# Optimization experiments

Measured on AMD Instinct MI355X. Metric: run time of the kernel, lower is better.

The kernel has to match this reference:

```python
import jax, jax.numpy as jnp
import numpy as np

EPS = 1e-5

def layer_norm(x, gamma, beta):
    mu = jnp.mean(x, axis=-1, keepdims=True)
    var = jnp.var(x, axis=-1, keepdims=True)
    return (x - mu) * jax.lax.rsqrt(var + EPS) * gamma + beta

def setup_inputs() -> dict:
    key = jax.random.key(0)
    ks = jax.random.split(key, 8)
    B, S, D, OUT = 32768, 6, 128, 1024
    return {
        "x": jax.random.normal(ks[0], (B, S, D), dtype=jnp.float32),
        "W_qkv": jax.random.normal(ks[1], (D, 3 * D), dtype=jnp.float32) * 0.02,
        "b_qkv": jnp.zeros((3 * D,), dtype=jnp.float32),
        "g1": jnp.ones((256,), dtype=jnp.float32),
        "be1": jnp.zeros((256,), dtype=jnp.float32),
        "W_fp": jax.random.normal(ks[2], (256, 256), dtype=jnp.float32) * 0.02,
        "b_fp": jnp.zeros((256,), dtype=jnp.float32),
        "g2": jnp.ones((512,), dtype=jnp.float32),
        "be2": jnp.zeros((512,), dtype=jnp.float32),
        "W_s": jax.random.normal(ks[3], (S * 512, OUT), dtype=jnp.float32) * 0.02,
        "b_s": jnp.zeros((OUT,), dtype=jnp.float32),
    }

def reference(x, W_qkv, b_qkv, g1, be1, W_fp, b_fp, g2, be2, W_s, b_s):
    D = 128
    qkv = x @ W_qkv + b_qkv                      # [B,6,384]
    Q, K, V = qkv[..., :D], qkv[..., D:2*D], qkv[..., 2*D:]
    # attention WITHOUT softmax, as in the original module
    attn = jnp.einsum('bqd,bkd->bqk', Q, K)      # [B,6,6]
    attn_result = jnp.einsum('bqk,bkd->bqd', attn, V)  # [B,6,128]
    m = jnp.concatenate([x, attn_result], axis=2)      # [B,6,256]
    n = layer_norm(m, g1, be1)
    n = n @ W_fp + b_fp                          # [B,6,256]
    f = jnp.concatenate([n, m], axis=2)          # [B,6,512]
    f = layer_norm(f, g2, be2)
    f = f.reshape(-1, 6 * 512)                   # [B,3072]
    out = jax.nn.relu(f @ W_s + b_s)             # [B,1024]
    return out
```

## Files before the change

### kernel.cpp

```cpp
#include <hip/hip_runtime.h>
#include <stdint.h>

typedef short bf16x8 __attribute__((ext_vector_type(8)));
typedef float f32x4 __attribute__((ext_vector_type(4)));

__device__ __forceinline__ float bf2f(uint16_t b){
  union { uint32_t u; float f; } v; v.u = ((uint32_t)b) << 16; return v.f;
}
__device__ __forceinline__ float u2f(uint32_t u){
  union { uint32_t u; float f; } v; v.u = u; return v.f;
}
__device__ __forceinline__ uint16_t f2bf(float f){
  union { float f; uint32_t u; } v; v.f = f;
  uint32_t u = v.u;
  return (uint16_t)((u + 0x7FFFu + ((u >> 16) & 1u)) >> 16);
}

__device__ __forceinline__ void gl2lds16(const uint16_t* g, uint16_t* l) {
  __builtin_amdgcn_global_load_lds((const __attribute__((address_space(1))) void*)g,
                                   (__attribute__((address_space(3))) void*)l, 16, 0, 0);
}

__global__ __launch_bounds__(256) void transpose_cvt(
    const float* __restrict__ src, uint16_t* __restrict__ dst, int K, int N)
{
  __shared__ float tile[32][33];
  int n0 = blockIdx.x * 32, k0 = blockIdx.y * 32;
  int tx = threadIdx.x & 31, ty = threadIdx.x >> 5;
  #pragma unroll
  for (int i = 0; i < 4; i++)
    tile[ty + 8*i][tx] = src[(size_t)(k0 + ty + 8*i) * N + n0 + tx];
  __syncthreads();
  #pragma unroll
  for (int i = 0; i < 4; i++)
    dst[(size_t)(n0 + ty + 8*i) * K + k0 + tx] = f2bf(tile[tx][ty + 8*i]);
}

#define LX 136
#define LQ 392
#define LNM 264

__global__ __launch_bounds__(256) void fused_mid(
    const float* __restrict__ X, const uint16_t* __restrict__ WqkvT,
    const float* __restrict__ bqkv, const float* __restrict__ g1,
    const float* __restrict__ be1, const uint16_t* __restrict__ WfpT,
    const float* __restrict__ bfp, const float* __restrict__ g2,
    const float* __restrict__ be2, uint16_t* __restrict__ F)
{
  __shared__ uint16_t xs[48 * LX];
  __shared__ uint16_t qs[48 * LQ];
  __shared__ uint16_t nm[48 * LNM];
  __shared__ float    sb[8 * 36];
  __shared__ float    smu[48], srs[48];
  int t = threadIdx.x;
  int lane = t & 63, wave = t >> 6;
  int lr = lane & 15, lh = lane >> 4;
  size_t r0 = (size_t)blockIdx.x * 48;

  for (int i = t; i < 768; i += 256) {
    int row = i >> 4, c = (i & 15) * 8;
    const float* g = X + (r0 + row) * 128 + c;
    f32x4 v0 = *(const f32x4*)g, v1 = *(const f32x4*)(g + 4);
    bf16x8 o;
    #pragma unroll
    for (int j = 0; j < 4; j++) { o[j] = (short)f2bf(v0[j]); o[4+j] = (short)f2bf(v1[j]); }
    *(bf16x8*)(xs + row * LX + c) = o;
  }
  __syncthreads();

  {
    f32x4 acc[3][6] = {};
    #pragma unroll
    for (int k0 = 0; k0 < 128; k0 += 32) {
      bf16x8 af[3], bw[6];
      #pragma unroll
      for (int i = 0; i < 3; i++)
        af[i] = *(const bf16x8*)(xs + (i*16 + lr) * LX + k0 + lh*8);
      #pragma unroll
      for (int j = 0; j < 6; j++)
        bw[j] = *(const bf16x8*)(WqkvT + (size_t)(wave*96 + j*16 + lr) * 128 + k0 + lh*8);
      #pragma unroll
      for (int i = 0; i < 3; i++)
        #pragma unroll
        for (int j = 0; j < 6; j++)
          acc[i][j] = __builtin_amdgcn_mfma_f32_16x16x32_bf16(af[i], bw[j], acc[i][j], 0, 0, 0);
    }
    #pragma unroll
    for (int i = 0; i < 3; i++)
      #pragma unroll
      for (int j = 0; j < 6; j++) {
        int col = wave*96 + j*16 + lr;
        float bv = bqkv[col];
        #pragma unroll
        for (int r = 0; r < 4; r++)
          qs[(i*16 + lh*4 + r) * LQ + col] = f2bf(acc[i][j][r] + bv);
      }
  }
  __syncthreads();

  for (int i = t; i < 288; i += 256) {
    int b = i / 36, q = (i / 6) % 6, k = i % 6;
    const uint32_t* Qr = (const uint32_t*)(qs + (b*6 + q) * LQ);
    const uint32_t* Kr = (const uint32_t*)(qs + (b*6 + k) * LQ + 128);
    float s = 0.f;
    #pragma unroll 8
    for (int d = 0; d < 64; d++) {
      uint32_t qu = Qr[d], ku = Kr[d];
      s += u2f(qu << 16) * u2f(ku << 16) + u2f(qu & 0xFFFF0000u) * u2f(ku & 0xFFFF0000u);
    }
    sb[i] = s;
  }
  __syncthreads();

  for (int i = t; i < 3072; i += 256) {
    int r = i >> 6, dp = i & 63;
    int b = r / 6;
    const float* sr = sb + b*36 + (r - b*6)*6;
    float a0 = 0.f, a1 = 0.f;
    #pragma unroll
    for (int k = 0; k < 6; k++) {
      uint32_t vu = *(const uint32_t*)(qs + (b*6 + k)*LQ + 256 + dp*2);
      a0 += sr[k] * u2f(vu << 16);
      a1 += sr[k] * u2f(vu & 0xFFFF0000u);
    }
    *((uint32_t*)(qs + r*LQ) + dp) = (uint32_t)f2bf(a0) | ((uint32_t)f2bf(a1) << 16);
  }
  __syncthreads();

  if (t < 192) {
    int r = t >> 2, p = t & 3;
    const uint32_t* src = (p < 2) ? (const uint32_t*)(xs + r*LX + p*64)
                                  : (const uint32_t*)(qs + r*LQ + (p - 2)*64);
    float s1 = 0.f, s2 = 0.f;
    #pragma unroll 8
    for (int d = 0; d < 32; d++) {
      uint32_t u = src[d];
      float a = u2f(u << 16), b = u2f(u & 0xFFFF0000u);
      s1 += a + b; s2 += a*a + b*b;
    }
    s1 += __shfl_xor(s1, 1); s2 += __shfl_xor(s2, 1);
    s1 += __shfl_xor(s1, 2); s2 += __shfl_xor(s2, 2);
    float mu = s1 * (1.f/256.f);
    float var = s2 * (1.f/256.f) - mu*mu;
    if (p == 0) { smu[r] = mu; srs[r] = rsqrtf(var + 1e-5f); }
  }
  __syncthreads();

  for (int i = t; i < 1536; i += 256) {
    int r = i >> 5, c0 = (i & 31) * 8;
    float mu = smu[r], rs = srs[r];
    const uint16_t* src = (c0 < 128) ? (xs + r*LX + c0) : (qs + r*LQ + (c0 - 128));
    bf16x8 v = *(const bf16x8*)src;
    bf16x8 o;
    #pragma unroll
    for (int j = 0; j < 8; j++)
      o[j] = (short)f2bf((bf2f((uint16_t)v[j]) - mu) * rs * g1[c0+j] + be1[c0+j]);
    *(bf16x8*)(nm + r*LNM + c0) = o;
  }
  __syncthreads();

  f32x4 acc2[3][4] = {};
  #pragma unroll
  for (int k0 = 0; k0 < 256; k0 += 32) {
    bf16x8 af[3], bw[4];
    #pragma unroll
    for (int i = 0; i < 3; i++)
      af[i] = *(const bf16x8*)(nm + (i*16 + lr) * LNM + k0 + lh*8);
    #pragma unroll
    for (int j = 0; j < 4; j++)
      bw[j] = *(const bf16x8*)(WfpT + (size_t)(wave*64 + j*16 + lr) * 256 + k0 + lh*8);
    #pragma unroll
    for (int i = 0; i < 3; i++)
      #pragma unroll
      for (int j = 0; j < 4; j++)
        acc2[i][j] = __builtin_amdgcn_mfma_f32_16x16x32_bf16(af[i], bw[j], acc2[i][j], 0, 0, 0);
  }
  __syncthreads();

  #pragma unroll
  for (int i = 0; i < 3; i++)
    #pragma unroll
    for (int j = 0; j < 4; j++) {
      int col = wave*64 + j*16 + lr;
      float bv = bfp[col];
      #pragma unroll
      for (int r = 0; r < 4; r++)
        nm[(i*16 + lh*4 + r) * LNM + col] = f2bf(acc2[i][j][r] + bv);
    }
  __syncthreads();

  if (t < 192) {
    int r = t >> 2, p = t & 3;
    const uint32_t* src = (p < 2) ? (const uint32_t*)(nm + r*LNM + p*128)
                        : (p == 2) ? (const uint32_t*)(xs + r*LX)
                                   : (const uint32_t*)(qs + r*LQ);
    float s1 = 0.f, s2 = 0.f;
    #pragma unroll 8
    for (int d = 0; d < 64; d++) {
      uint32_t u = src[d];
      float a = u2f(u << 16), b = u2f(u & 0xFFFF0000u);
      s1 += a + b; s2 += a*a + b*b;
    }
    s1 += __shfl_xor(s1, 1); s2 += __shfl_xor(s2, 1);
    s1 += __shfl_xor(s1, 2); s2 += __shfl_xor(s2, 2);
    float mu = s1 * (1.f/512.f);
    float var = s2 * (1.f/512.f) - mu*mu;
    if (p == 0) { smu[r] = mu; srs[r] = rsqrtf(var + 1e-5f); }
  }
  __syncthreads();

  for (int i = t; i < 3072; i += 256) {
    int r = i >> 6, c0 = (i & 63) * 8;
    float mu = smu[r], rs = srs[r];
    const uint16_t* src = (c0 < 256) ? (nm + r*LNM + c0)
                        : (c0 < 384) ? (xs + r*LX + (c0 - 256))
                                     : (qs + r*LQ + (c0 - 384));
    bf16x8 v = *(const bf16x8*)src;
    bf16x8 o;
    #pragma unroll
    for (int j = 0; j < 8; j++)
      o[j] = (short)f2bf((bf2f((uint16_t)v[j]) - mu) * rs * g2[c0+j] + be2[c0+j]);
    *(bf16x8*)(F + (r0 + r) * 512 + c0) = o;
  }
}

__global__ __launch_bounds__(512, 2) void out_gemm(
    const uint16_t* __restrict__ F, const uint16_t* __restrict__ WsT,
    const float* __restrict__ b_s, float* __restrict__ OUT)
{
  __shared__ uint16_t lds[3][2][256*32];
  int t = threadIdx.x;
  int lane = t & 63, wave = t >> 6;
  int wm = wave >> 2, wn = wave & 3;
  int lr = lane & 15, lh = lane >> 4;

  int bid = blockIdx.x;
  int swz = (bid & 7) * 64 + (bid >> 3);
  size_t m0 = (size_t)(swz >> 2) * 256;
  int n0 = (swz & 3) * 256;

  int srow = t >> 2;
  int gch  = (t & 3) ^ ((t >> 3) & 3);
  const uint16_t* Ag = F   + (m0 + srow) * 3072 + gch * 8;
  const uint16_t* Bg = WsT + (size_t)(n0 + srow) * 3072 + gch * 8;

#define STAGE(s, tt) do {                                                    \
    int kk0 = (tt) * 32;                                                     \
    uint16_t* la = &lds[s][0][0];                                            \
    uint16_t* lb = &lds[s][1][0];                                            \
    gl2lds16(Ag + kk0,                    la + wave*512);                    \
    gl2lds16(Ag + (size_t)128*3072 + kk0, la + 4096 + wave*512);             \
    gl2lds16(Bg + kk0,                    lb + wave*512);                    \
    gl2lds16(Bg + (size_t)128*3072 + kk0, lb + 4096 + wave*512);             \
  } while(0)

  f32x4 acc[8][4] = {};
  int swch = (lh ^ ((lr >> 1) & 3)) * 8;

#define COMPUTE(s) do {                                                      \
    const uint16_t* As_ = &lds[s][0][0];                                     \
    const uint16_t* Bs_ = &lds[s][1][0];                                     \
    bf16x8 af[8], bfr[4];                                                    \
    _Pragma("unroll")                                                        \
    for (int i = 0; i < 8; i++)                                              \
      af[i]  = *(const bf16x8*)(As_ + (wm*128 + i*16 + lr)*32 + swch);       \
    _Pragma("unroll")                                                        \
    for (int j = 0; j < 4; j++)                                              \
      bfr[j] = *(const bf16x8*)(Bs_ + (wn*64 + j*16 + lr)*32 + swch);        \
    __builtin_amdgcn_s_setprio(1);                                           \
    _Pragma("unroll")                                                        \
    for (int i = 0; i < 8; i++)                                              \
      _Pragma("unroll")                                                      \
      for (int j = 0; j < 4; j++)                                            \
        acc[i][j] = __builtin_amdgcn_mfma_f32_16x16x32_bf16(af[i], bfr[j],   \
                                                            acc[i][j],0,0,0);\
    __builtin_amdgcn_s_setprio(0);                                           \
  } while(0)

  STAGE(0, 0);
  STAGE(1, 1);
  int ss = 2, sc = 0;
  for (int tt = 0; tt < 94; ++tt) {
    asm volatile("s_waitcnt vmcnt(4)" ::: "memory");
    __builtin_amdgcn_s_barrier();
    asm volatile("" ::: "memory");
    STAGE(ss, tt + 2);
    COMPUTE(sc);
    ss = (ss == 2) ? 0 : ss + 1;
    sc = (sc == 2) ? 0 : sc + 1;
  }
  asm volatile("s_waitcnt vmcnt(4)" ::: "memory");
  __builtin_amdgcn_s_barrier();
  asm volatile("" ::: "memory");
  COMPUTE(1);
  asm volatile("s_waitcnt vmcnt(0)" ::: "memory");
  __builtin_amdgcn_s_barrier();
  asm volatile("" ::: "memory");
  COMPUTE(2);

#undef STAGE
#undef COMPUTE

  #pragma unroll
  for (int i = 0; i < 8; i++)
    #pragma unroll
    for (int j = 0; j < 4; j++) {
      int col = n0 + wn*64 + j*16 + lr;
      float bv = b_s[col];
      #pragma unroll
      for (int r = 0; r < 4; r++) {
        size_t row = m0 + wm*128 + i*16 + lh*4 + r;
        OUT[row * 1024 + col] = fmaxf(acc[i][j][r] + bv, 0.f);
      }
    }
}

extern "C" void kernel_launch(void* const* d_in, const int* in_sizes, int n_in,
                              void* d_out, int out_size, void* d_ws, size_t ws_size,
                              hipStream_t stream) {
  const float* x    = (const float*)d_in[0];
  const float* Wqkv = (const float*)d_in[1];
  const float* bqkv = (const float*)d_in[2];
  const float* g1   = (const float*)d_in[3];
  const float* be1  = (const float*)d_in[4];
  const float* Wfp  = (const float*)d_in[5];
  const float* bfp  = (const float*)d_in[6];
  const float* g2   = (const float*)d_in[7];
  const float* be2  = (const float*)d_in[8];
  const float* Ws   = (const float*)d_in[9];
  const float* bs   = (const float*)d_in[10];
  float* out = (float*)d_out;

  uint8_t* ws = (uint8_t*)d_ws;
  uint16_t* F     = (uint16_t*)(ws);
  uint16_t* WqkvT = (uint16_t*)(ws + 201326592ull);
  uint16_t* WfpT  = (uint16_t*)(ws + 201424896ull);
  uint16_t* WsT   = (uint16_t*)(ws + 201555968ull);

  transpose_cvt<<<dim3(12, 4), 256, 0, stream>>>(Wqkv, WqkvT, 128, 384);
  transpose_cvt<<<dim3(8, 8), 256, 0, stream>>>(Wfp, WfpT, 256, 256);
  transpose_cvt<<<dim3(32, 96), 256, 0, stream>>>(Ws, WsT, 3072, 1024);
  fused_mid<<<dim3(4096), 256, 0, stream>>>(x, WqkvT, bqkv, g1, be1,
                                            WfpT, bfp, g2, be2, F);
  out_gemm<<<dim3(512), 512, 0, stream>>>(F, WsT, bs, out);
}
```

Baseline: 426.6 us.

## Fold LayerNorm1 affine into Wfp and use packed bf16 conversion

Folds the first LayerNorm's gamma into the Wfp weights and its mean, rstd and beta into a per-column correction applied in the GEMM epilogue. This lets the second GEMM read the raw concatenated activations straight from LDS, removing a normalize pass and a barrier. It also swaps the manual bf16 rounding for the hardware v_cvt_pk_bf16_f32 packed conversion and vectorizes the gamma/beta loads in the last LayerNorm. The folding applies the normalization after bf16 rounding, so results can differ numerically (cancellation in the mean-times-column-sum term), and a single-block fold kernel is added.

```diff
diff --git a/kernel.cpp b/kernel.cpp
--- a/kernel.cpp
+++ b/kernel.cpp
@@ -3,6 +3,7 @@
 
 typedef short bf16x8 __attribute__((ext_vector_type(8)));
 typedef float f32x4 __attribute__((ext_vector_type(4)));
+typedef uint32_t u32x4 __attribute__((ext_vector_type(4)));
 
 __device__ __forceinline__ float bf2f(uint16_t b){
   union { uint32_t u; float f; } v; v.u = ((uint32_t)b) << 16; return v.f;
@@ -10,10 +11,13 @@
 __device__ __forceinline__ float u2f(uint32_t u){
   union { uint32_t u; float f; } v; v.u = u; return v.f;
 }
+__device__ __forceinline__ uint32_t pk_bf16(float a, float b){
+  uint32_t r;
+  asm("v_cvt_pk_bf16_f32 %0, %1, %2" : "=v"(r) : "v"(a), "v"(b));
+  return r;
+}
 __device__ __forceinline__ uint16_t f2bf(float f){
-  union { float f; uint32_t u; } v; v.f = f;
-  uint32_t u = v.u;
-  return (uint16_t)((u + 0x7FFFu + ((u >> 16) & 1u)) >> 16);
+  return (uint16_t)pk_bf16(f, f);
 }
 
 __device__ __forceinline__ void gl2lds16(const uint16_t* g, uint16_t* l) {
@@ -22,18 +26,39 @@
 }
 
 __global__ __launch_bounds__(256) void transpose_cvt(
-    const float* __restrict__ src, uint16_t* __restrict__ dst, int K, int N)
+    const float* __restrict__ src, uint16_t* __restrict__ dst, int K, int N,
+    const float* __restrict__ scale)
 {
   __shared__ float tile[32][33];
   int n0 = blockIdx.x * 32, k0 = blockIdx.y * 32;
   int tx = threadIdx.x & 31, ty = threadIdx.x >> 5;
   #pragma unroll
-  for (int i = 0; i < 4; i++)
-    tile[ty + 8*i][tx] = src[(size_t)(k0 + ty + 8*i) * N + n0 + tx];
+  for (int i = 0; i < 4; i++) {
+    int k = k0 + ty + 8*i;
+    float v = src[(size_t)k * N + n0 + tx];
+    if (scale) v *= scale[k];
+    tile[ty + 8*i][tx] = v;
+  }
   __syncthreads();
   #pragma unroll
   for (int i = 0; i < 4; i++)
     dst[(size_t)(n0 + ty + 8*i) * K + k0 + tx] = f2bf(tile[tx][ty + 8*i]);
+}
+
+__global__ __launch_bounds__(256) void fold_fp(
+    const float* __restrict__ Wfp, const float* __restrict__ g1,
+    const float* __restrict__ be1, const float* __restrict__ bfp,
+    float* __restrict__ c1, float* __restrict__ b1p)
+{
+  int j = threadIdx.x;
+  float c = 0.f, b = 0.f;
+  for (int k = 0; k < 256; k++) {
+    float w = Wfp[k * 256 + j];
+    c += g1[k] * w;
+    b += be1[k] * w;
+  }
+  c1[j] = c;
+  b1p[j] = b + bfp[j];
 }
 
 #define LX 136
@@ -42,10 +67,10 @@
 
 __global__ __launch_bounds__(256) void fused_mid(
     const float* __restrict__ X, const uint16_t* __restrict__ WqkvT,
-    const float* __restrict__ bqkv, const float* __restrict__ g1,
-    const float* __restrict__ be1, const uint16_t* __restrict__ WfpT,
-    const float* __restrict__ bfp, const float* __restrict__ g2,
-    const float* __restrict__ be2, uint16_t* __restrict__ F)
+    const float* __restrict__ bqkv, const uint16_t* __restrict__ Wfp2T,
+    const float* __restrict__ c1, const float* __restrict__ b1p,
+    const float* __restrict__ g2, const float* __restrict__ be2,
+    uint16_t* __restrict__ F)
 {
   __shared__ uint16_t xs[48 * LX];
   __shared__ uint16_t qs[48 * LQ];
@@ -61,10 +86,10 @@
     int row = i >> 4, c = (i & 15) * 8;
     const float* g = X + (r0 + row) * 128 + c;
     f32x4 v0 = *(const f32x4*)g, v1 = *(const f32x4*)(g + 4);
-    bf16x8 o;
-    #pragma unroll
-    for (int j = 0; j < 4; j++) { o[j] = (short)f2bf(v0[j]); o[4+j] = (short)f2bf(v1[j]); }
-    *(bf16x8*)(xs + row * LX + c) = o;
+    u32x4 o;
+    o[0] = pk_bf16(v0[0], v0[1]); o[1] = pk_bf16(v0[2], v0[3]);
+    o[2] = pk_bf16(v1[0], v1[1]); o[3] = pk_bf16(v1[2], v1[3]);
+    *(u32x4*)(xs + row * LX + c) = o;
   }
   __syncthreads();
 
@@ -123,7 +148,7 @@
       a0 += sr[k] * u2f(vu << 16);
       a1 += sr[k] * u2f(vu & 0xFFFF0000u);
     }
-    *((uint32_t*)(qs + r*LQ) + dp) = (uint32_t)f2bf(a0) | ((uint32_t)f2bf(a1) << 16);
+    *((uint32_t*)(qs + r*LQ) + dp) = pk_bf16(a0, a1);
   }
   __syncthreads();
 
@@ -144,31 +169,19 @@
     float var = s2 * (1.f/256.f) - mu*mu;
     if (p == 0) { smu[r] = mu; srs[r] = rsqrtf(var + 1e-5f); }
   }
-  __syncthreads();
-
-  for (int i = t; i < 1536; i += 256) {
-    int r = i >> 5, c0 = (i & 31) * 8;
-    float mu = smu[r], rs = srs[r];
-    const uint16_t* src = (c0 < 128) ? (xs + r*LX + c0) : (qs + r*LQ + (c0 - 128));
-    bf16x8 v = *(const bf16x8*)src;
-    bf16x8 o;
-    #pragma unroll
-    for (int j = 0; j < 8; j++)
-      o[j] = (short)f2bf((bf2f((uint16_t)v[j]) - mu) * rs * g1[c0+j] + be1[c0+j]);
-    *(bf16x8*)(nm + r*LNM + c0) = o;
-  }
-  __syncthreads();
-
   f32x4 acc2[3][4] = {};
   #pragma unroll
   for (int k0 = 0; k0 < 256; k0 += 32) {
     bf16x8 af[3], bw[4];
     #pragma unroll
-    for (int i = 0; i < 3; i++)
-      af[i] = *(const bf16x8*)(nm + (i*16 + lr) * LNM + k0 + lh*8);
+    for (int i = 0; i < 3; i++) {
+      const uint16_t* mrow = (k0 < 128) ? (xs + (i*16 + lr) * LX + k0)
+                                        : (qs + (i*16 + lr) * LQ + (k0 - 128));
+      af[i] = *(const bf16x8*)(mrow + lh*8);
+    }
     #pragma unroll
     for (int j = 0; j < 4; j++)
-      bw[j] = *(const bf16x8*)(WfpT + (size_t)(wave*64 + j*16 + lr) * 256 + k0 + lh*8);
+      bw[j] = *(const bf16x8*)(Wfp2T + (size_t)(wave*64 + j*16 + lr) * 256 + k0 + lh*8);
     #pragma unroll
     for (int i = 0; i < 3; i++)
       #pragma unroll
@@ -182,10 +195,13 @@
     #pragma unroll
     for (int j = 0; j < 4; j++) {
       int col = wave*64 + j*16 + lr;
-      float bv = bfp[col];
-      #pragma unroll
-      for (int r = 0; r < 4; r++)
-        nm[(i*16 + lh*4 + r) * LNM + col] = f2bf(acc2[i][j][r] + bv);
+      float c1v = c1[col], b1v = b1p[col];
+      #pragma unroll
+      for (int r = 0; r < 4; r++) {
+        int row = i*16 + lh*4 + r;
+        float h = srs[row] * (acc2[i][j][r] - smu[row] * c1v) + b1v;
+        nm[row * LNM + col] = f2bf(h);
+      }
     }
   __syncthreads();
 
@@ -216,11 +232,18 @@
                         : (c0 < 384) ? (xs + r*LX + (c0 - 256))
                                      : (qs + r*LQ + (c0 - 384));
     bf16x8 v = *(const bf16x8*)src;
-    bf16x8 o;
-    #pragma unroll
-    for (int j = 0; j < 8; j++)
-      o[j] = (short)f2bf((bf2f((uint16_t)v[j]) - mu) * rs * g2[c0+j] + be2[c0+j]);
-    *(bf16x8*)(F + (r0 + r) * 512 + c0) = o;
+    f32x4 gv0 = *(const f32x4*)(g2 + c0), gv1 = *(const f32x4*)(g2 + c0 + 4);
+    f32x4 bv0 = *(const f32x4*)(be2 + c0), bv1 = *(const f32x4*)(be2 + c0 + 4);
+    float f[8];
+    #pragma unroll
+    for (int j = 0; j < 4; j++) {
+      f[j]   = (bf2f((uint16_t)v[j])   - mu) * rs * gv0[j] + bv0[j];
+      f[4+j] = (bf2f((uint16_t)v[4+j]) - mu) * rs * gv1[j] + bv1[j];
+    }
+    u32x4 o;
+    o[0] = pk_bf16(f[0], f[1]); o[1] = pk_bf16(f[2], f[3]);
+    o[2] = pk_bf16(f[4], f[5]); o[3] = pk_bf16(f[6], f[7]);
+    *(u32x4*)(F + (r0 + r) * 512 + c0) = o;
   }
 }
 
@@ -334,13 +357,16 @@
   uint8_t* ws = (uint8_t*)d_ws;
   uint16_t* F     = (uint16_t*)(ws);
   uint16_t* WqkvT = (uint16_t*)(ws + 201326592ull);
-  uint16_t* WfpT  = (uint16_t*)(ws + 201424896ull);
+  uint16_t* Wfp2T = (uint16_t*)(ws + 201424896ull);
   uint16_t* WsT   = (uint16_t*)(ws + 201555968ull);
-
-  transpose_cvt<<<dim3(12, 4), 256, 0, stream>>>(Wqkv, WqkvT, 128, 384);
-  transpose_cvt<<<dim3(8, 8), 256, 0, stream>>>(Wfp, WfpT, 256, 256);
-  transpose_cvt<<<dim3(32, 96), 256, 0, stream>>>(Ws, WsT, 3072, 1024);
-  fused_mid<<<dim3(4096), 256, 0, stream>>>(x, WqkvT, bqkv, g1, be1,
-                                            WfpT, bfp, g2, be2, F);
+  float*    c1    = (float*)(ws + 207847424ull);
+  float*    b1p   = (float*)(ws + 207848448ull);
+
+  transpose_cvt<<<dim3(12, 4), 256, 0, stream>>>(Wqkv, WqkvT, 128, 384, nullptr);
+  transpose_cvt<<<dim3(8, 8), 256, 0, stream>>>(Wfp, Wfp2T, 256, 256, g1);
+  transpose_cvt<<<dim3(32, 96), 256, 0, stream>>>(Ws, WsT, 3072, 1024, nullptr);
+  fold_fp<<<dim3(1), 256, 0, stream>>>(Wfp, g1, be1, bfp, c1, b1p);
+  fused_mid<<<dim3(4096), 256, 0, stream>>>(x, WqkvT, bqkv, Wfp2T, c1, b1p,
+                                            g2, be2, F);
   out_gemm<<<dim3(512), 512, 0, stream>>>(F, WsT, bs, out);
 }
```

Result: no change. 433.0 us (+1.5%).
